# Kernel tuning notes

Measured on AMD Instinct MI355X. Metric: run time of the kernel, lower is better.

## Reference

```python
import jax, jax.numpy as jnp
import numpy as np

N_NODES = 2048
N_RELS = 16
N_FEAT = 256
N_EDGES = 262144


def setup_inputs() -> dict:
    key = jax.random.key(0)
    k1, k2, k3, k4, k5, k6 = jax.random.split(key, 6)
    x = jax.random.normal(k1, (N_NODES, N_FEAT), dtype=jnp.float32)
    relations = jax.random.normal(k2, (N_RELS, N_FEAT), dtype=jnp.float32)
    outer_weight = jax.random.normal(k3, (N_FEAT,), dtype=jnp.float32)
    src = jax.random.randint(k4, (N_EDGES,), 0, N_NODES, dtype=jnp.int64)
    rel = jax.random.randint(k5, (N_EDGES,), 0, N_RELS, dtype=jnp.int64)
    dst = jax.random.randint(k6, (N_EDGES,), 0, N_NODES, dtype=jnp.int64)
    edge_index = jnp.stack([src, rel, dst])  # [3, E]
    return {"x": x, "relations": relations, "outer_weight": outer_weight,
            "edge_index": edge_index}


def reference(x, relations, outer_weight, edge_index):
    # R[r] = outer(relations[r], outer_weight)  -> [R, F, F]
    R = relations[:, :, None] * outer_weight[None, None, :]
    # adj = x @ R @ x^T  -> [R, N, N] (faithful dense materialization)
    adj = jnp.einsum('nf,rfg,mg->rnm', x, R, x)
    adj = jax.nn.sigmoid(adj)
    # gather per-edge scores: adj[rel, src, dst]
    return adj[edge_index[1], edge_index[0], edge_index[2]]
```

## Files before the change

### kernel.cpp

```cpp
#include <hip/hip_runtime.h>
#include <math.h>

#define N_NODES 2048
#define N_RELS 16
#define N_FEAT 256

__global__ void precompute_kernel(const float* __restrict__ x,
                                  const float* __restrict__ relations,
                                  const float* __restrict__ outer_weight,
                                  float* __restrict__ A,
                                  float* __restrict__ B)
{
    const int n = blockIdx.x;
    const int lane = threadIdx.x;

    const float4 xv = reinterpret_cast<const float4*>(x + n * N_FEAT)[lane];
    const float4 wv = reinterpret_cast<const float4*>(outer_weight)[lane];

    float b = xv.x * wv.x + xv.y * wv.y + xv.z * wv.z + xv.w * wv.w;
    #pragma unroll
    for (int off = 32; off > 0; off >>= 1) b += __shfl_xor(b, off, 64);
    if (lane == 0) B[n] = b;

    #pragma unroll
    for (int r = 0; r < N_RELS; ++r) {
        const float4 rv =
            reinterpret_cast<const float4*>(relations + r * N_FEAT)[lane];
        float a = xv.x * rv.x + xv.y * rv.y + xv.z * rv.z + xv.w * rv.w;
        #pragma unroll
        for (int off = 32; off > 0; off >>= 1) a += __shfl_xor(a, off, 64);
        if (lane == 0) A[r * N_NODES + n] = a;
    }
}

__device__ __forceinline__ float sigmoidf_fast(float z) {
    return 1.0f / (1.0f + __expf(-z));
}

__global__ void edge_kernel(const int* __restrict__ src,
                            const int* __restrict__ rel,
                            const int* __restrict__ dst,
                            const float* __restrict__ A,
                            const float* __restrict__ B,
                            float* __restrict__ out,
                            int E)
{
    const int t = blockIdx.x * blockDim.x + threadIdx.x;
    const int e4 = t * 4;
    if (e4 + 3 < E) {
        const int4 s = *reinterpret_cast<const int4*>(src + e4);
        const int4 r = *reinterpret_cast<const int4*>(rel + e4);
        const int4 d = *reinterpret_cast<const int4*>(dst + e4);
        float4 o;
        o.x = sigmoidf_fast(A[r.x * N_NODES + s.x] * B[d.x]);
        o.y = sigmoidf_fast(A[r.y * N_NODES + s.y] * B[d.y]);
        o.z = sigmoidf_fast(A[r.z * N_NODES + s.z] * B[d.z]);
        o.w = sigmoidf_fast(A[r.w * N_NODES + s.w] * B[d.w]);
        *reinterpret_cast<float4*>(out + e4) = o;
    } else {
        for (int e = e4; e < E; ++e) {
            out[e] = sigmoidf_fast(A[rel[e] * N_NODES + src[e]] * B[dst[e]]);
        }
    }
}

extern "C" void kernel_launch(void* const* d_in, const int* in_sizes, int n_in,
                              void* d_out, int out_size, void* d_ws, size_t ws_size,
                              hipStream_t stream) {
    const float* x            = (const float*)d_in[0];
    const float* relations    = (const float*)d_in[1];
    const float* outer_weight = (const float*)d_in[2];
    const int*   edge_index   = (const int*)d_in[3];

    const int E = in_sizes[3] / 3;
    const int* src = edge_index;
    const int* rel = edge_index + E;
    const int* dst = edge_index + 2 * E;

    float* A = (float*)d_ws;
    float* B = A + N_RELS * N_NODES;

    precompute_kernel<<<N_NODES, 64, 0, stream>>>(x, relations, outer_weight, A, B);

    const int threads = 256;
    const int work = (E + 3) / 4;
    const int blocks = (work + threads - 1) / threads;
    edge_kernel<<<blocks, threads, 0, stream>>>(src, rel, dst, A, B,
                                                (float*)d_out, E);
}
```

Before: 15.27 us.

## Parallelize precompute across node-relation pairs and use nontemporal 2-wide edge loads

The precompute kernel now gives each wavefront a single (node, relation-or-weight) dot product, 2048*17 wavefronts in total, instead of one wavefront serially computing 17 reductions per node. This is meant to raise parallelism and shorten the per-wave serial chain, at the cost of reloading each x row 17 times. The edge kernel now handles 2 edges per thread instead of 4 and uses nontemporal loads and stores for the streaming index and output arrays. That doubles the thread count and aims to cut cache pollution so the gathered A and B tables stay resident.

After: 12.86 us. 1.19x faster.

```diff
diff --git a/kernel.cpp b/kernel.cpp
--- a/kernel.cpp
+++ b/kernel.cpp
@@ -2,65 +2,76 @@
 #include <math.h>
 
 #define N_NODES 2048
-#define N_RELS 16
-#define N_FEAT 256
+#define N_RELS  16
+#define N_FEAT  256
+#define N_JOBS  (N_RELS + 1)
+#define THREADS 256
 
-__global__ void precompute_kernel(const float* __restrict__ x,
-                                  const float* __restrict__ relations,
-                                  const float* __restrict__ outer_weight,
-                                  float* __restrict__ A,
-                                  float* __restrict__ B)
-{
-    const int n = blockIdx.x;
-    const int lane = threadIdx.x;
-
-    const float4 xv = reinterpret_cast<const float4*>(x + n * N_FEAT)[lane];
-    const float4 wv = reinterpret_cast<const float4*>(outer_weight)[lane];
-
-    float b = xv.x * wv.x + xv.y * wv.y + xv.z * wv.z + xv.w * wv.w;
-    #pragma unroll
-    for (int off = 32; off > 0; off >>= 1) b += __shfl_xor(b, off, 64);
-    if (lane == 0) B[n] = b;
-
-    #pragma unroll
-    for (int r = 0; r < N_RELS; ++r) {
-        const float4 rv =
-            reinterpret_cast<const float4*>(relations + r * N_FEAT)[lane];
-        float a = xv.x * rv.x + xv.y * rv.y + xv.z * rv.z + xv.w * rv.w;
-        #pragma unroll
-        for (int off = 32; off > 0; off >>= 1) a += __shfl_xor(a, off, 64);
-        if (lane == 0) A[r * N_NODES + n] = a;
-    }
-}
+typedef int   v2i __attribute__((ext_vector_type(2)));
+typedef float v2f __attribute__((ext_vector_type(2)));
 
 __device__ __forceinline__ float sigmoidf_fast(float z) {
     return 1.0f / (1.0f + __expf(-z));
 }
 
-__global__ void edge_kernel(const int* __restrict__ src,
-                            const int* __restrict__ rel,
-                            const int* __restrict__ dst,
-                            const float* __restrict__ A,
-                            const float* __restrict__ B,
-                            float* __restrict__ out,
-                            int E)
+__global__ void __launch_bounds__(THREADS)
+precompute_kernel(const float* __restrict__ x,
+                  const float* __restrict__ relations,
+                  const float* __restrict__ outer_weight,
+                  float* __restrict__ A,
+                  float* __restrict__ B)
 {
-    const int t = blockIdx.x * blockDim.x + threadIdx.x;
-    const int e4 = t * 4;
-    if (e4 + 3 < E) {
-        const int4 s = *reinterpret_cast<const int4*>(src + e4);
-        const int4 r = *reinterpret_cast<const int4*>(rel + e4);
-        const int4 d = *reinterpret_cast<const int4*>(dst + e4);
-        float4 o;
-        o.x = sigmoidf_fast(A[r.x * N_NODES + s.x] * B[d.x]);
-        o.y = sigmoidf_fast(A[r.y * N_NODES + s.y] * B[d.y]);
-        o.z = sigmoidf_fast(A[r.z * N_NODES + s.z] * B[d.z]);
-        o.w = sigmoidf_fast(A[r.w * N_NODES + s.w] * B[d.w]);
-        *reinterpret_cast<float4*>(out + e4) = o;
-    } else {
-        for (int e = e4; e < E; ++e) {
+    const int t    = blockIdx.x * blockDim.x + threadIdx.x;
+    const int w    = t >> 6;
+    const int lane = t & 63;
+    if (w >= N_NODES * N_JOBS) return;
+
+    const int n = w / N_JOBS;
+    const int j = w - n * N_JOBS;
+
+    const float4 xv = reinterpret_cast<const float4*>(x + n * N_FEAT)[lane];
+    const float* rbase = (j < N_RELS) ? (relations + j * N_FEAT) : outer_weight;
+    const float4 rv = reinterpret_cast<const float4*>(rbase)[lane];
+
+    float a = xv.x * rv.x + xv.y * rv.y + xv.z * rv.z + xv.w * rv.w;
+    #pragma unroll
+    for (int off = 32; off > 0; off >>= 1) a += __shfl_xor(a, off, 64);
+
+    if (lane == 0) {
+        if (j < N_RELS) A[j * N_NODES + n] = a;
+        else            B[n] = a;
+    }
+}
+
+__global__ void __launch_bounds__(THREADS)
+edge_kernel(const int* __restrict__ src,
+            const int* __restrict__ rel,
+            const int* __restrict__ dst,
+            const float* __restrict__ A,
+            const float* __restrict__ B,
+            float* __restrict__ out,
+            int E)
+{
+    const int t  = blockIdx.x * blockDim.x + threadIdx.x;
+    const int e2 = t * 2;
+    if (e2 + 1 < E) {
+        const v2i s = __builtin_nontemporal_load(
+            reinterpret_cast<const v2i*>(src + e2));
+        const v2i r = __builtin_nontemporal_load(
+            reinterpret_cast<const v2i*>(rel + e2));
+        const v2i d = __builtin_nontemporal_load(
+            reinterpret_cast<const v2i*>(dst + e2));
+        const float a0 = A[r.x * N_NODES + s.x];
+        const float a1 = A[r.y * N_NODES + s.y];
+        const float b0 = B[d.x];
+        const float b1 = B[d.y];
+        v2f o;
+        o.x = sigmoidf_fast(a0 * b0);
+        o.y = sigmoidf_fast(a1 * b1);
+        __builtin_nontemporal_store(o, reinterpret_cast<v2f*>(out + e2));
+    } else if (e2 < E) {
+        for (int e = e2; e < E; ++e)
             out[e] = sigmoidf_fast(A[rel[e] * N_NODES + src[e]] * B[dst[e]]);
-        }
     }
 }
 
@@ -80,11 +91,13 @@
     float* A = (float*)d_ws;
     float* B = A + N_RELS * N_NODES;
 
-    precompute_kernel<<<N_NODES, 64, 0, stream>>>(x, relations, outer_weight, A, B);
+    const int total_pre_threads = N_NODES * N_JOBS * 64;
+    const int pre_blocks = (total_pre_threads + THREADS - 1) / THREADS;
+    precompute_kernel<<<pre_blocks, THREADS, 0, stream>>>(
+        x, relations, outer_weight, A, B);
 
-    const int threads = 256;
-    const int work = (E + 3) / 4;
-    const int blocks = (work + threads - 1) / threads;
-    edge_kernel<<<blocks, threads, 0, stream>>>(src, rel, dst, A, B,
-                                                (float*)d_out, E);
+    const int work = (E + 1) / 2;
+    const int edge_blocks = (work + THREADS - 1) / THREADS;
+    edge_kernel<<<edge_blocks, THREADS, 0, stream>>>(
+        src, rel, dst, A, B, (float*)d_out, E);
 }
```
